# Kernel tuning notes

Measured on AMD Instinct MI355X. Metric: run time of the kernel, lower is better.

Reference implementation:

```python
import jax, jax.numpy as jnp
import numpy as np

NUM_HEADS = 2
POOL_K = 256
REPEAT = 20


def setup_inputs() -> dict:
    key = jax.random.key(0)
    k1, k2, k3 = jax.random.split(key, 3)
    C = 6144
    d = C // NUM_HEADS                      # 3072
    N = REPEAT * (d // POOL_K)              # 240, required by Pq add
    x = jax.random.normal(k1, (N, C), dtype=jnp.float32)
    w_qkv = jax.random.normal(k2, (3 * C, C), dtype=jnp.float32) * 0.02
    w_proj = jax.random.normal(k3, (C, C), dtype=jnp.float32) * 0.02
    b_proj = jnp.zeros((C,), dtype=jnp.float32)
    return {"x": x, "w_qkv": w_qkv, "w_proj": w_proj, "b_proj": b_proj}


def reference(x, w_qkv, w_proj, b_proj):
    N, C = x.shape
    H = NUM_HEADS
    d = C // H
    scale = d ** -0.5
    # qkv: (N, 3C) -> (N, 3, H, d) -> (3, H, N, d)
    qkv = (x @ w_qkv.T).reshape(N, 3, H, d).transpose(1, 2, 0, 3)
    q, k, v = qkv[0], qkv[1], qkv[2]        # each (H, N, d)
    # MaxPool1d(256) over last dim, then tile x20 along last dim -> (H, N, N)
    Pq = q.reshape(H, N, d // POOL_K, POOL_K).max(axis=-1)
    Pq = jnp.tile(Pq, (1, 1, REPEAT))       # (H, N, N)
    attn = jnp.einsum('hnd,hmd->hnm', q, k) * scale + 0.1 * Pq
    attn = jax.nn.softmax(attn, axis=-1)
    out = jnp.einsum('hnm,hmd->hnd', attn, v)    # (H, N, d)
    out = out.transpose(1, 0, 2).reshape(N, C)
    return out @ w_proj.T + b_proj
```

## Files before the change

### kernel.cpp

```cpp
#include <hip/hip_runtime.h>
#include <hip/hip_bf16.h>

#define NN 240
#define CC 6144
#define DD 3072
#define C3 18432
#define HH 2

typedef __attribute__((ext_vector_type(8))) short bf16x8;
typedef __attribute__((ext_vector_type(4))) float f32x4;
typedef unsigned short ushort_t;

static __device__ __forceinline__ unsigned short f2bf(float f) {
    __hip_bfloat16 h = __float2bfloat16(f);
    return __builtin_bit_cast(unsigned short, h);
}

#define GLDS16(g, l) __builtin_amdgcn_global_load_lds( \
    (const __attribute__((address_space(1))) void*)(g), \
    (__attribute__((address_space(3))) void*)(l), 16, 0, 0)

__global__ __launch_bounds__(256, 4)
void gemm_m97(const ushort_t* __restrict__ Ab, int lda, long long sAz,
              const float* __restrict__ B, int ldb, long long sBz,
              const float* __restrict__ bias,
              float* __restrict__ C0, long long sC0z,
              float* __restrict__ CP, long long sCPz,
              int ldc, int N, int Kc, int KS) {
    __shared__ ushort_t sA[256 * 32];
    __shared__ float    sB[64 * 32];

    const int zc = blockIdx.z;
    const int z = zc / KS, kc = zc % KS;
    const ushort_t* Abase = Ab + (size_t)z * sAz + (size_t)kc * Kc;
    const float*    Bbase = B  + (size_t)z * sBz + (size_t)kc * Kc;
    float* Cw = (kc == 0) ? (C0 + (size_t)z * sC0z)
                          : (CP + (size_t)(z * (KS - 1) + kc - 1) * sCPz);

    const int n0 = blockIdx.x * 64;
    const int tid = threadIdx.x, lane = tid & 63, wid = tid >> 6;
    const int l16 = lane & 15, lk = lane >> 4;

    const int ar = lane >> 2;
    const int akoct = (lane & 3) ^ ((lane >> 3) & 3);

    long long bofs[2];
#pragma unroll
    for (int i = 0; i < 2; ++i) {
        int cl = (wid * 2 + i) * 8 + (lane >> 3);
        int cg = n0 + cl; if (cg > N - 1) cg = N - 1;
        bofs[i] = (long long)cg * ldb + ((lane & 7) ^ ((lane >> 3) & 7)) * 4;
    }

    const int nt = Kc / 32;
    f32x4 acc[4][4] = {};

    for (int t = 0; t < nt; ++t) {
#pragma unroll
        for (int i = 0; i < 4; ++i) {
            int rb = (wid * 4 + i) * 16;
            GLDS16(Abase + (size_t)(rb + ar) * lda + akoct * 8 + (size_t)t * 32,
                   sA + rb * 32);
        }
#pragma unroll
        for (int i = 0; i < 2; ++i) {
            int cb = (wid * 2 + i) * 8;
            GLDS16(Bbase + bofs[i] + (size_t)t * 32, sB + cb * 32);
        }
        __syncthreads();

        bf16x8 af[4];
#pragma unroll
        for (int mt = 0; mt < 4; ++mt) {
            int r = wid * 64 + mt * 16 + l16;
            af[mt] = *(const bf16x8*)((const char*)sA + r * 64
                        + ((lk ^ ((r >> 1) & 3)) * 16));
        }
#pragma unroll
        for (int nf = 0; nf < 4; ++nf) {
            int c = nf * 16 + l16;
            const char* cb = (const char*)sB + c * 128;
            f32x4 lo = *(const f32x4*)(cb + (((2 * lk) ^ (c & 7)) * 16));
            f32x4 hi = *(const f32x4*)(cb + (((2 * lk + 1) ^ (c & 7)) * 16));
            bf16x8 r;
            r[0] = (short)f2bf(lo[0]); r[1] = (short)f2bf(lo[1]);
            r[2] = (short)f2bf(lo[2]); r[3] = (short)f2bf(lo[3]);
            r[4] = (short)f2bf(hi[0]); r[5] = (short)f2bf(hi[1]);
            r[6] = (short)f2bf(hi[2]); r[7] = (short)f2bf(hi[3]);
#pragma unroll
            for (int mt = 0; mt < 4; ++mt)
                acc[mt][nf] = __builtin_amdgcn_mfma_f32_16x16x32_bf16(
                    af[mt], r, acc[mt][nf], 0, 0, 0);
        }
        __syncthreads();
    }

#pragma unroll
    for (int mt = 0; mt < 4; ++mt) {
#pragma unroll
        for (int j = 0; j < 4; ++j) {
            int grow = wid * 64 + mt * 16 + lk * 4 + j;
            if (grow < NN) {
#pragma unroll
                for (int nf = 0; nf < 4; ++nf) {
                    int gcol = n0 + nf * 16 + l16;
                    if (gcol < N) {
                        float v = acc[mt][nf][j];
                        if (kc == 0 && bias) v += bias[gcol];
                        Cw[(size_t)grow * ldc + gcol] = v;
                    }
                }
            }
        }
    }
}

__global__ __launch_bounds__(256)
void convert_kernel(const float* __restrict__ x, ushort_t* __restrict__ xb) {
    int id = blockIdx.x * 256 + threadIdx.x;
    int row = id / 768, c8 = id % 768;
    bf16x8 o = {};
    if (row < NN) {
        const float* p = x + (size_t)row * CC + c8 * 8;
        float4 a = *(const float4*)p, b = *(const float4*)(p + 4);
        o[0] = (short)f2bf(a.x); o[1] = (short)f2bf(a.y);
        o[2] = (short)f2bf(a.z); o[3] = (short)f2bf(a.w);
        o[4] = (short)f2bf(b.x); o[5] = (short)f2bf(b.y);
        o[6] = (short)f2bf(b.z); o[7] = (short)f2bf(b.w);
    }
    *(bf16x8*)(xb + (size_t)row * CC + c8 * 8) = o;
}

__global__ __launch_bounds__(256)
void reduce_qkv(float4* __restrict__ q4, const float4* __restrict__ p4,
                ushort_t* __restrict__ qb) {
    int i = blockIdx.x * 256 + threadIdx.x;
    float4 a = q4[i], b = p4[i];
    a.x += b.x; a.y += b.y; a.z += b.z; a.w += b.w;
    q4[i] = a;
    int row = i / 4608, c4 = i % 4608;
    if (c4 < 1536) {
        ushort4 u;
        u.x = f2bf(a.x); u.y = f2bf(a.y); u.z = f2bf(a.z); u.w = f2bf(a.w);
        *(ushort4*)(qb + (size_t)row * CC + c4 * 4) = u;
    }
}

__global__ __launch_bounds__(256)
void reduce_proj(float4* __restrict__ o4, const float4* __restrict__ p4,
                 long long s4) {
    int i = blockIdx.x * 256 + threadIdx.x;
    float4 a = o4[i];
#pragma unroll
    for (int k = 0; k < 7; ++k) {
        float4 b = p4[(size_t)k * s4 + i];
        a.x += b.x; a.y += b.y; a.z += b.z; a.w += b.w;
    }
    o4[i] = a;
}

__global__ __launch_bounds__(256)
void qmax_kernel(const float* __restrict__ qkv, float* __restrict__ qmax) {
    int idx = blockIdx.x * 4 + (threadIdx.x >> 6);
    int lane = threadIdx.x & 63;
    int c = idx % 12;
    int r = idx / 12;
    int n = r % NN, h = r / NN;
    const float* p = qkv + (size_t)n * C3 + h * DD + c * 256 + lane * 4;
    float4 f = *(const float4*)p;
    float m = fmaxf(fmaxf(f.x, f.y), fmaxf(f.z, f.w));
#pragma unroll
    for (int off = 32; off >= 1; off >>= 1)
        m = fmaxf(m, __shfl_xor(m, off));
    if (lane == 0) qmax[idx] = m;
}

__global__ __launch_bounds__(256)
void softmax_kernel(float* __restrict__ attn, const float* __restrict__ gpart,
                    int ksm1, const float* __restrict__ qmax) {
    int r = blockIdx.x * 4 + (threadIdx.x >> 6);
    int lane = threadIdx.x & 63;
    int z = r / NN, n = r % NN;
    float* row = attn + (size_t)r * NN;
    const float* qm = qmax + r * 12;
    const float scale = 0.0180421959f;
    float v[4];
    float mx = -1e30f;
#pragma unroll
    for (int i = 0; i < 4; ++i) {
        int m = lane + 64 * i;
        v[i] = -1e30f;
        if (m < NN) {
            float s = row[m];
            for (int kc = 0; kc < ksm1; ++kc)
                s += gpart[(size_t)(z * ksm1 + kc) * (NN * NN)
                           + (size_t)n * NN + m];
            v[i] = s * scale + 0.1f * qm[m % 12];
        }
        mx = fmaxf(mx, v[i]);
    }
#pragma unroll
    for (int off = 32; off >= 1; off >>= 1)
        mx = fmaxf(mx, __shfl_xor(mx, off));
    float s = 0.f;
#pragma unroll
    for (int i = 0; i < 4; ++i) {
        v[i] = __expf(v[i] - mx);
        s += v[i];
    }
#pragma unroll
    for (int off = 32; off >= 1; off >>= 1)
        s += __shfl_xor(s, off);
    float inv = 1.0f / s;
#pragma unroll
    for (int i = 0; i < 4; ++i) {
        int m = lane + 64 * i;
        if (m < NN) row[m] = v[i] * inv;
    }
}

__global__ __launch_bounds__(256)
void pv_kernel(const float* __restrict__ attn, const float* __restrict__ qkv,
               ushort_t* __restrict__ preb) {
    const int h = blockIdx.z;
    const int n0 = blockIdx.y * 16;
    const int dd0 = blockIdx.x * 256;
    __shared__ float s_attn[16 * NN];
    for (int i = threadIdx.x; i < 16 * NN; i += 256)
        s_attn[i] = attn[(size_t)h * NN * NN + (n0 + i / NN) * NN + (i % NN)];
    __syncthreads();

    const float* vp = qkv + 2 * CC + h * DD + dd0 + threadIdx.x;
    float acc[16] = {};
    for (int m = 0; m < NN; m += 4) {
        float v0 = vp[(size_t)(m + 0) * C3];
        float v1 = vp[(size_t)(m + 1) * C3];
        float v2 = vp[(size_t)(m + 2) * C3];
        float v3 = vp[(size_t)(m + 3) * C3];
#pragma unroll
        for (int i = 0; i < 16; ++i) {
            float4 a = *(const float4*)&s_attn[i * NN + m];
            acc[i] += a.x * v0 + a.y * v1 + a.z * v2 + a.w * v3;
        }
    }
#pragma unroll
    for (int i = 0; i < 16; ++i)
        preb[(size_t)(n0 + i) * CC + h * DD + dd0 + threadIdx.x] =
            f2bf(acc[i]);
}

extern "C" void kernel_launch(void* const* d_in, const int* in_sizes, int n_in,
                              void* d_out, int out_size, void* d_ws, size_t ws_size,
                              hipStream_t stream) {
    const float* x      = (const float*)d_in[0];
    const float* w_qkv  = (const float*)d_in[1];
    const float* w_proj = (const float*)d_in[2];
    const float* b_proj = (const float*)d_in[3];
    float* out = (float*)d_out;

    const size_t f_qkv  = (size_t)NN * C3;
    const size_t f_attn = (size_t)HH * NN * NN;
    const size_t f_qmax = (size_t)HH * NN * 12;
    const size_t f_pre  = (size_t)NN * CC;
    float* qkv   = (float*)d_ws;
    float* attn  = qkv + f_qkv;
    float* qmaxb = attn + f_attn;
    ushort_t* xb   = (ushort_t*)(qmaxb + f_qmax);
    ushort_t* qb   = xb + (size_t)256 * CC;
    ushort_t* preb = qb + (size_t)256 * CC;
    float* gpart = (float*)(preb + (size_t)256 * CC);

    convert_kernel<<<768, 256, 0, stream>>>(x, xb);

    gemm_m97<<<dim3(C3 / 64, 1, 2), 256, 0, stream>>>(
        xb, CC, 0LL, w_qkv, CC, 0LL, nullptr,
        qkv, 0LL, gpart, (long long)f_qkv,
        C3, C3, CC / 2, 2);
    reduce_qkv<<<4320, 256, 0, stream>>>((float4*)qkv, (const float4*)gpart, qb);

    qmax_kernel<<<1440, 256, 0, stream>>>(qkv, qmaxb);

    gemm_m97<<<dim3(4, 1, HH * 24), 256, 0, stream>>>(
        qb, CC, (long long)DD,
        qkv + CC, C3, (long long)DD, nullptr,
        attn, (long long)(NN * NN), gpart, (long long)(NN * NN),
        NN, NN, DD / 24, 24);

    softmax_kernel<<<120, 256, 0, stream>>>(attn, gpart, 23, qmaxb);

    pv_kernel<<<dim3(12, 15, HH), 256, 0, stream>>>(attn, qkv, preb);

    gemm_m97<<<dim3(CC / 64, 1, 8), 256, 0, stream>>>(
        preb, CC, 0LL, w_proj, CC, 0LL, b_proj,
        out, 0LL, gpart, (long long)f_pre,
        CC, CC, CC / 8, 8);
    reduce_proj<<<1440, 256, 0, stream>>>((float4*)out, (const float4*)gpart,
        (long long)(f_pre / 4));
}
```

Before: 369.0 us.

## Add narrow-N GEMM with wide B staging, drop qkv split-K and reduce pass

Adds a new GEMM kernel with 32-column tiles that stages 256 K-values of the fp32 weight operand in LDS at a time, refilling it every eight 32-wide A steps. The QKV projection now runs without split-K over 576 blocks and writes the bf16 copy of Q directly in its epilogue, which removes the reduce_qkv kernel and its partial-buffer traffic. The output projection drops from 8-way to 4-way split-K, so reduce_proj reads fewer partials. The trade-off is fewer blocks with longer K loops, plus a larger LDS footprint that limits occupancy to 2 blocks per CU, and the B staging is not double-buffered.

```diff
diff --git a/kernel.cpp b/kernel.cpp
--- a/kernel.cpp
+++ b/kernel.cpp
@@ -20,10 +20,112 @@
     (const __attribute__((address_space(1))) void*)(g), \
     (__attribute__((address_space(3))) void*)(l), 16, 0, 0)
 
+__global__ __launch_bounds__(256, 2)
+void gemm_pb(const ushort_t* __restrict__ Ab, int lda,
+             const float* __restrict__ B, int ldb,
+             const float* __restrict__ bias,
+             float* __restrict__ C0,
+             float* __restrict__ CP, long long sCPz,
+             int ldc, int N, int Kc, int KS,
+             ushort_t* __restrict__ Qb) {
+    __shared__ ushort_t sA[256 * 32];
+    __shared__ float    sB[32 * 256];
+
+    const int kc = blockIdx.z;
+    const ushort_t* Abase = Ab + (size_t)kc * Kc;
+    const float*    Bbase = B  + (size_t)kc * Kc;
+    float* Cw = (kc == 0) ? C0 : (CP + (size_t)(kc - 1) * sCPz);
+
+    const int n0 = blockIdx.x * 32;
+    const int tid = threadIdx.x, lane = tid & 63, wid = tid >> 6;
+    const int l16 = lane & 15, lk = lane >> 4;
+
+    const int ar = lane >> 2;
+    const int akoct = (lane & 3) ^ ((lane >> 3) & 3);
+
+    const int nTot = Kc / 32;
+    f32x4 acc[4][2] = {};
+
+    auto ISSUE_A = [&](int t32) {
+#pragma unroll
+        for (int i = 0; i < 4; ++i) {
+            int rb = (wid * 4 + i) * 16;
+            GLDS16(Abase + (size_t)(rb + ar) * lda + akoct * 8
+                       + (size_t)t32 * 32,
+                   sA + rb * 32);
+        }
+    };
+    auto ISSUE_B = [&](int T) {
+#pragma unroll
+        for (int i = 0; i < 8; ++i) {
+            int c = wid * 8 + i;
+            const float* src = Bbase + (size_t)(n0 + c) * ldb
+                               + (size_t)T * 256 + (lane ^ i) * 4;
+            GLDS16(src, sB + c * 256);
+        }
+    };
+    auto COMPUTE = [&](int s) {
+        bf16x8 af[4];
+#pragma unroll
+        for (int mt = 0; mt < 4; ++mt) {
+            int r = wid * 64 + mt * 16 + l16;
+            af[mt] = *(const bf16x8*)((const char*)sA + r * 64
+                        + ((lk ^ ((r >> 1) & 3)) * 16));
+        }
+#pragma unroll
+        for (int nf = 0; nf < 2; ++nf) {
+            int c = nf * 16 + l16;
+            int j0 = (s * 8 + 2 * lk) ^ (c & 7);
+            int j1 = (s * 8 + 2 * lk + 1) ^ (c & 7);
+            f32x4 lo = *(const f32x4*)(sB + c * 256 + j0 * 4);
+            f32x4 hi = *(const f32x4*)(sB + c * 256 + j1 * 4);
+            bf16x8 r;
+            r[0] = (short)f2bf(lo[0]); r[1] = (short)f2bf(lo[1]);
+            r[2] = (short)f2bf(lo[2]); r[3] = (short)f2bf(lo[3]);
+            r[4] = (short)f2bf(hi[0]); r[5] = (short)f2bf(hi[1]);
+            r[6] = (short)f2bf(hi[2]); r[7] = (short)f2bf(hi[3]);
+#pragma unroll
+            for (int mt = 0; mt < 4; ++mt)
+                acc[mt][nf] = __builtin_amdgcn_mfma_f32_16x16x32_bf16(
+                    af[mt], r, acc[mt][nf], 0, 0, 0);
+        }
+    };
+
+    ISSUE_B(0);
+    for (int t = 0; t < nTot; ++t) {
+        ISSUE_A(t);
+        __syncthreads();
+        COMPUTE(t & 7);
+        __syncthreads();
+        if ((t & 7) == 7 && t + 1 < nTot)
+            ISSUE_B((t >> 3) + 1);
+    }
+
+#pragma unroll
+    for (int mt = 0; mt < 4; ++mt) {
+#pragma unroll
+        for (int j = 0; j < 4; ++j) {
+            int grow = wid * 64 + mt * 16 + lk * 4 + j;
+            if (grow < NN) {
+#pragma unroll
+                for (int nf = 0; nf < 2; ++nf) {
+                    int gcol = n0 + nf * 16 + l16;
+                    if (gcol < N) {
+                        float v = acc[mt][nf][j];
+                        if (kc == 0 && bias) v += bias[gcol];
+                        Cw[(size_t)grow * ldc + gcol] = v;
+                        if (Qb && gcol < CC)
+                            Qb[(size_t)grow * CC + gcol] = f2bf(v);
+                    }
+                }
+            }
+        }
+    }
+}
+
 __global__ __launch_bounds__(256, 4)
 void gemm_m97(const ushort_t* __restrict__ Ab, int lda, long long sAz,
               const float* __restrict__ B, int ldb, long long sBz,
-              const float* __restrict__ bias,
               float* __restrict__ C0, long long sC0z,
               float* __restrict__ CP, long long sCPz,
               int ldc, int N, int Kc, int KS) {
@@ -104,11 +206,8 @@
 #pragma unroll
                 for (int nf = 0; nf < 4; ++nf) {
                     int gcol = n0 + nf * 16 + l16;
-                    if (gcol < N) {
-                        float v = acc[mt][nf][j];
-                        if (kc == 0 && bias) v += bias[gcol];
-                        Cw[(size_t)grow * ldc + gcol] = v;
-                    }
+                    if (gcol < N)
+                        Cw[(size_t)grow * ldc + gcol] = acc[mt][nf][j];
                 }
             }
         }
@@ -132,27 +231,12 @@
 }
 
 __global__ __launch_bounds__(256)
-void reduce_qkv(float4* __restrict__ q4, const float4* __restrict__ p4,
-                ushort_t* __restrict__ qb) {
-    int i = blockIdx.x * 256 + threadIdx.x;
-    float4 a = q4[i], b = p4[i];
-    a.x += b.x; a.y += b.y; a.z += b.z; a.w += b.w;
-    q4[i] = a;
-    int row = i / 4608, c4 = i % 4608;
-    if (c4 < 1536) {
-        ushort4 u;
-        u.x = f2bf(a.x); u.y = f2bf(a.y); u.z = f2bf(a.z); u.w = f2bf(a.w);
-        *(ushort4*)(qb + (size_t)row * CC + c4 * 4) = u;
-    }
-}
-
-__global__ __launch_bounds__(256)
 void reduce_proj(float4* __restrict__ o4, const float4* __restrict__ p4,
                  long long s4) {
     int i = blockIdx.x * 256 + threadIdx.x;
     float4 a = o4[i];
 #pragma unroll
-    for (int k = 0; k < 7; ++k) {
+    for (int k = 0; k < 3; ++k) {
         float4 b = p4[(size_t)k * s4 + i];
         a.x += b.x; a.y += b.y; a.z += b.z; a.w += b.w;
     }
@@ -272,17 +356,16 @@
 
     convert_kernel<<<768, 256, 0, stream>>>(x, xb);
 
-    gemm_m97<<<dim3(C3 / 64, 1, 2), 256, 0, stream>>>(
-        xb, CC, 0LL, w_qkv, CC, 0LL, nullptr,
-        qkv, 0LL, gpart, (long long)f_qkv,
-        C3, C3, CC / 2, 2);
-    reduce_qkv<<<4320, 256, 0, stream>>>((float4*)qkv, (const float4*)gpart, qb);
+    gemm_pb<<<dim3(C3 / 32, 1, 1), 256, 0, stream>>>(
+        xb, CC, w_qkv, CC, nullptr,
+        qkv, nullptr, 0LL,
+        C3, C3, CC, 1, qb);
 
     qmax_kernel<<<1440, 256, 0, stream>>>(qkv, qmaxb);
 
     gemm_m97<<<dim3(4, 1, HH * 24), 256, 0, stream>>>(
         qb, CC, (long long)DD,
-        qkv + CC, C3, (long long)DD, nullptr,
+        qkv + CC, C3, (long long)DD,
         attn, (long long)(NN * NN), gpart, (long long)(NN * NN),
         NN, NN, DD / 24, 24);
 
@@ -290,10 +373,10 @@
 
     pv_kernel<<<dim3(12, 15, HH), 256, 0, stream>>>(attn, qkv, preb);
 
-    gemm_m97<<<dim3(CC / 64, 1, 8), 256, 0, stream>>>(
-        preb, CC, 0LL, w_proj, CC, 0LL, b_proj,
-        out, 0LL, gpart, (long long)f_pre,
-        CC, CC, CC / 8, 8);
+    gemm_pb<<<dim3(CC / 32, 1, 4), 256, 0, stream>>>(
+        preb, CC, w_proj, CC, b_proj,
+        out, gpart, (long long)f_pre,
+        CC, CC, CC / 4, 4, nullptr);
     reduce_proj<<<1440, 256, 0, stream>>>((float4*)out, (const float4*)gpart,
         (long long)(f_pre / 4));
 }
```

Result: faster. 350.9 us (-4.9%).
